# Optimization experiments

Measured on AMD Instinct MI355X. Metric: run time of the kernel, lower is better.

The kernel has to match this reference:

```python
import jax, jax.numpy as jnp
import numpy as np

HEADS = 16

def setup_inputs() -> dict:
    key = jax.random.key(0)
    ks = jax.random.split(key, 5)
    B, N, C = 2, 2048, 1024
    s = 0.02
    return {
        "x": jax.random.normal(ks[0], (B, N, C), jnp.float32),
        "y": jax.random.normal(ks[1], (B, N, C), jnp.float32),
        "w_qkv": jax.random.normal(ks[2], (C, 3 * C), jnp.float32) * s,  # acts as Linear weight^T
        "w_proj": jax.random.normal(ks[3], (C, C), jnp.float32) * s,
        "b_proj": jnp.zeros((C,), jnp.float32),
    }

def _qkv_heads(t, w_qkv, B, N, H, D):
    qkv = (t @ w_qkv).reshape(B, N, 3, H, D)
    qkv = jnp.transpose(qkv, (2, 0, 3, 1, 4))  # [3, B, H, N, D]
    return qkv[0], qkv[1], qkv[2]

def reference(x, y, w_qkv, w_proj, b_proj):
    B, N, C = x.shape
    H = HEADS
    D = C // H
    scale = D ** (-0.5)
    q, k, v = _qkv_heads(x, w_qkv, B, N, H, D)
    q1, k1, v1 = _qkv_heads(y, w_qkv, B, N, H, D)
    attn = jax.nn.softmax(jnp.einsum('bhnd,bhmd->bhnm', q, k) * scale, axis=-1)
    attn1 = jax.nn.softmax(jnp.einsum('bhnd,bhmd->bhnm', q1, k1) * scale, axis=-1)
    # cross-swapped values: x-branch attends over v1 (from y), y-branch over v (from x)
    ox = jnp.einsum('bhnm,bhmd->bhnd', attn, v1)
    oy = jnp.einsum('bhnm,bhmd->bhnd', attn1, v)
    ox = jnp.transpose(ox, (0, 2, 1, 3)).reshape(B, N, C)
    oy = jnp.transpose(oy, (0, 2, 1, 3)).reshape(B, N, C)
    x_out = ox @ w_proj + b_proj + x
    y_out = oy @ w_proj + b_proj + y
    return x_out, y_out
```

## Files before the change

kernel.cpp:

```cpp
#include <hip/hip_runtime.h>

using u16    = unsigned short;
using short8 = __attribute__((ext_vector_type(8))) short;
using f32x4  = __attribute__((ext_vector_type(4))) float;
using f32x16 = __attribute__((ext_vector_type(16))) float;

#define MFMA16(a, b, c) __builtin_amdgcn_mfma_f32_16x16x32_bf16(a, b, c, 0, 0, 0)
#define MFMA32(a, b, c) __builtin_amdgcn_mfma_f32_32x32x16_bf16(a, b, c, 0, 0, 0)

#define QSCALE 0.18033688011112042f

__device__ inline u16 f2bf(float f) {
  union { float f; unsigned u; } v; v.f = f;
  unsigned r = v.u + 0x7fffu + ((v.u >> 16) & 1u);
  return (u16)(r >> 16);
}

__device__ __forceinline__ void load_lds16(const u16* g, u16* l) {
  __builtin_amdgcn_global_load_lds((const __attribute__((address_space(1))) void*)g,
                                   (__attribute__((address_space(3))) void*)l, 16, 0, 0);
}

__device__ __forceinline__ unsigned cvt_pk_bf16(float lo, float hi) {
  unsigned r;
  asm("v_cvt_pk_bf16_f32 %0, %1, %2" : "=v"(r) : "v"(lo), "v"(hi));
  return r;
}

__device__ __forceinline__ void plswap(unsigned& a, unsigned& b) {
  auto r = __builtin_amdgcn_permlane32_swap(a, b, false, false);
  a = r[0];
  b = r[1];
}

__global__ __launch_bounds__(256) void cvt2_k(const float* __restrict__ s0,
                                              const float* __restrict__ s1,
                                              u16* __restrict__ d0,
                                              u16* __restrict__ d1) {
  const float* src = blockIdx.y ? s1 : s0;
  u16* dst = blockIdx.y ? d1 : d0;
  const int i = (blockIdx.x * 256 + threadIdx.x) * 8;
  const float4 a = *(const float4*)&src[i];
  const float4 b = *(const float4*)&src[i + 4];
  short8 o;
  o[0] = (short)f2bf(a.x); o[1] = (short)f2bf(a.y);
  o[2] = (short)f2bf(a.z); o[3] = (short)f2bf(a.w);
  o[4] = (short)f2bf(b.x); o[5] = (short)f2bf(b.y);
  o[6] = (short)f2bf(b.z); o[7] = (short)f2bf(b.w);
  *(short8*)&dst[i] = o;
}

__global__ __launch_bounds__(256) void cvtT_k(const float* __restrict__ src,
                                              u16* __restrict__ dst, int R, int C) {
  __shared__ float t[64][65];
  const int c0 = blockIdx.x * 64, r0 = blockIdx.y * 64;
  const int lc = threadIdx.x & 63, g = threadIdx.x >> 6;
#pragma unroll
  for (int i = 0; i < 16; ++i) {
    const int r = g + i * 4;
    t[r][lc] = src[(size_t)(r0 + r) * C + c0 + lc];
  }
  __syncthreads();
#pragma unroll
  for (int i = 0; i < 16; ++i) {
    const int c = g + i * 4;
    dst[(size_t)(c0 + c) * R + r0 + lc] = f2bf(t[lc][c]);
  }
}

template <int MODE>
__global__ __launch_bounds__(256, 4) void gemm_k(
    const u16* __restrict__ A0, const u16* __restrict__ A1,
    const u16* __restrict__ Bt,
    u16* __restrict__ q_out, u16* __restrict__ k_out, u16* __restrict__ v_out,
    float* __restrict__ c0, float* __restrict__ c1,
    const float* __restrict__ bias,
    const float* __restrict__ res0, const float* __restrict__ res1) {
  __shared__ alignas(16) u16 lA[128 * 64];
  __shared__ alignas(16) u16 lB[128 * 64];

  const int nx = (MODE == 0) ? 24 : 8;
  const int nb = nx * 32 * 2;
  const int bi = blockIdx.x;
  const int L  = (bi & 7) * (nb >> 3) + (bi >> 3);
  const int xt = L % nx;
  const int yt = (L / nx) & 31;
  const int z  = L / (nx * 32);

  const u16* A = z ? A1 : A0;
  float* c_out = z ? c1 : c0;
  const float* res = z ? res1 : res0;
  const int head_base = z * 32;

  const int tid = threadIdx.x;
  const int lane = tid & 63, wave = tid >> 6;
  const int quad = lane >> 4, l16 = lane & 15;
  const int lsw = (l16 & 7) * 8;
  const int wm = (wave >> 1) * 64, wn = (wave & 1) * 64;
  const int bn0 = xt * 128, bm0 = yt * 128;
  const int srow = lane >> 3;
  const int sg = (lane & 7) ^ srow;

  f32x4 acc[4][4] = {};

  for (int k0 = 0; k0 < 1024; k0 += 64) {
    __syncthreads();
#pragma unroll
    for (int it = 0; it < 4; ++it) {
      const int rb = wave * 32 + it * 8;
      const int r = rb + srow;
      load_lds16(&A[(size_t)(bm0 + r) * 1024 + k0 + sg * 8], &lA[rb * 64]);
      load_lds16(&Bt[(size_t)(bn0 + r) * 1024 + k0 + sg * 8], &lB[rb * 64]);
    }
    asm volatile("s_waitcnt vmcnt(0)" ::: "memory");
    __syncthreads();
#pragma unroll
    for (int kt = 0; kt < 2; ++kt) {
      short8 af[4], bfr[4];
#pragma unroll
      for (int i = 0; i < 4; ++i) {
        const int go = ((kt * 4 + quad) * 8) ^ lsw;
        af[i]  = *(const short8*)&lA[(wm + i * 16 + l16) * 64 + go];
        bfr[i] = *(const short8*)&lB[(wn + i * 16 + l16) * 64 + go];
      }
#pragma unroll
      for (int i = 0; i < 4; ++i)
#pragma unroll
        for (int j = 0; j < 4; ++j)
          acc[i][j] = MFMA16(af[i], bfr[j], acc[i][j]);
    }
  }

#pragma unroll
  for (int i = 0; i < 4; ++i) {
    const int row = bm0 + wm + i * 16 + quad * 4;
#pragma unroll
    for (int j = 0; j < 4; ++j) {
      const int col = bn0 + wn + j * 16 + l16;
      if (MODE == 0) {
        const int which = col >> 10;
        const int h = (col >> 6) & 15, d = col & 63;
        const int b = row >> 11, n0 = row & 2047;
        const size_t hh = (size_t)(head_base + b * 16 + h);
        if (which == 2) {
          union { u16 pk[4]; uint2 v; } u;
#pragma unroll
          for (int r = 0; r < 4; ++r) u.pk[r] = f2bf(acc[i][j][r]);
          *(uint2*)&v_out[(hh * 64 + d) * 2048 + n0] = u.v;
        } else if (which == 0) {
#pragma unroll
          for (int r = 0; r < 4; ++r)
            q_out[(hh * 2048 + n0 + r) * 64 + d] = f2bf(acc[i][j][r] * QSCALE);
        } else {
#pragma unroll
          for (int r = 0; r < 4; ++r)
            k_out[(hh * 2048 + n0 + r) * 64 + d] = f2bf(acc[i][j][r]);
        }
      } else {
#pragma unroll
        for (int r = 0; r < 4; ++r) {
          const int m = row + r;
          const size_t idx = (size_t)m * 1024 + col;
          c_out[idx] = acc[i][j][r] + bias[col] + res[idx];
        }
      }
    }
  }
}

__global__ __launch_bounds__(256, 4) void attn_k(const u16* __restrict__ Q,
                                                 const u16* __restrict__ K,
                                                 const u16* __restrict__ V,
                                                 u16* __restrict__ O) {
  __shared__ alignas(16) u16 kT[2][64 * 64];
  __shared__ alignas(16) u16 vT[2][64 * 64];

  const int tid = threadIdx.x;
  const int lane = tid & 63, wave = tid >> 6;
  const int qn = lane & 31, h = lane >> 5;

  const int d0 = blockIdx.x;
  const int swz = ((d0 & 7) << 7) | (d0 >> 3);
  const int qx = swz & 15;
  const int hh = (swz >> 4) & 15;
  const int z  = swz >> 8;
  const int s = z >> 1, b = z & 1;

  const int head_qk = z * 16 + hh;
  const int head_v  = (z ^ 2) * 16 + hh;
  const u16* Qh = Q + (size_t)head_qk * 2048 * 64;
  const u16* Kh = K + (size_t)head_qk * 2048 * 64;
  const u16* Vh = V + (size_t)head_v * 64 * 2048;
  const int qr0 = qx * 128 + wave * 32;

  short8 qf[4];
#pragma unroll
  for (int f = 0; f < 4; ++f)
    qf[f] = *(const short8*)&Qh[(size_t)(qr0 + qn) * 64 + f * 16 + h * 8];

  short8 ones;
#pragma unroll
  for (int j = 0; j < 8; ++j) ones[j] = (short)0x3F80;

  f32x16 oacc[2] = {};
  f32x16 lacc = {};

  const int srow = lane >> 3;

  union PU { unsigned u[4]; short8 s; };

  auto stage = [&](int buf, int j0) {
#pragma unroll
    for (int it = 0; it < 2; ++it) {
      const int rb = wave * 16 + it * 8;
      const int r = rb + srow;
      const int sgx = (lane & 7) ^ srow ^ (rb >> 3);
      load_lds16(&Kh[(size_t)(j0 + r) * 64 + sgx * 8], &kT[buf][rb * 64]);
      load_lds16(&Vh[(size_t)r * 2048 + j0 + sgx * 8], &vT[buf][rb * 64]);
    }
  };

  stage(0, 0);
  asm volatile("s_waitcnt vmcnt(0)" ::: "memory");
  __syncthreads();

  int cur = 0;
  for (int j0 = 0; j0 < 2048; j0 += 64) {
    if (j0 + 64 < 2048) stage(cur ^ 1, j0 + 64);
    const u16* kb = kT[cur];
    const u16* vb = vT[cur];

    PU pa[4];
#pragma unroll
    for (int t = 0; t < 2; ++t) {
      f32x16 sacc = {};
      const int row = t * 32 + qn;
      const int key = (row & 7) ^ (row >> 3);
#pragma unroll
      for (int kd = 0; kd < 4; ++kd) {
        const int go = ((kd * 2 + h) ^ key) * 8;
        const short8 kf = *(const short8*)&kb[row * 64 + go];
        sacc = MFMA32(kf, qf[kd], sacc);
      }

      unsigned pw[8];
#pragma unroll
      for (int j = 0; j < 8; ++j) {
        const float p0 = __builtin_amdgcn_exp2f(sacc[2 * j]);
        const float p1 = __builtin_amdgcn_exp2f(sacc[2 * j + 1]);
        pw[j] = cvt_pk_bf16(p0, p1);
      }

#pragma unroll
      for (int e = 0; e < 2; ++e) {
        unsigned a0 = pw[4 * e + 0], a2 = pw[4 * e + 2];
        unsigned a1 = pw[4 * e + 1], a3 = pw[4 * e + 3];
        plswap(a0, a2);
        plswap(a1, a3);
        pa[2 * t + e].u[0] = a0; pa[2 * t + e].u[1] = a1;
        pa[2 * t + e].u[2] = a2; pa[2 * t + e].u[3] = a3;
      }
    }

#pragma unroll
    for (int st = 0; st < 4; ++st)
      lacc = MFMA32(pa[st].s, ones, lacc);

#pragma unroll
    for (int dt = 0; dt < 2; ++dt) {
      const int row = dt * 32 + qn;
      const int key = (row & 7) ^ (row >> 3);
#pragma unroll
      for (int st = 0; st < 4; ++st) {
        const int go = ((st * 2 + h) ^ key) * 8;
        const short8 vf = *(const short8*)&vb[row * 64 + go];
        oacc[dt] = MFMA32(pa[st].s, vf, oacc[dt]);
      }
    }

    asm volatile("s_waitcnt vmcnt(0)" ::: "memory");
    __syncthreads();
    cur ^= 1;
  }

  u16* Ob = O + (size_t)s * 4096 * 1024;
#pragma unroll
  for (int r = 0; r < 16; ++r) {
    const int qrow = (r & 3) + 8 * (r >> 2) + 4 * h;
    const float inv = 1.f / lacc[r];
    const size_t base = (size_t)(b * 2048 + qr0 + qrow) * 1024 + hh * 64;
#pragma unroll
    for (int dt = 0; dt < 2; ++dt)
      Ob[base + dt * 32 + qn] = f2bf(oacc[dt][r] * inv);
  }
}

extern "C" void kernel_launch(void* const* d_in, const int* in_sizes, int n_in,
                              void* d_out, int out_size, void* d_ws, size_t ws_size,
                              hipStream_t stream) {
  const float* x      = (const float*)d_in[0];
  const float* y      = (const float*)d_in[1];
  const float* w_qkv  = (const float*)d_in[2];
  const float* w_proj = (const float*)d_in[3];
  const float* b_proj = (const float*)d_in[4];
  float* out = (float*)d_out;

  u16* xb     = (u16*)d_ws;
  u16* yb     = xb + 4194304;
  u16* Ob     = xb;
  u16* wqkvT  = yb + 4194304;
  u16* wprojT = wqkvT + 3145728;
  u16* Qs     = wprojT + 1048576;
  u16* Ks     = Qs + 8388608;
  u16* Vs     = Ks + 8388608;

  cvt2_k<<<dim3(2048, 2), 256, 0, stream>>>(x, y, xb, yb);
  cvtT_k<<<dim3(48, 16), 256, 0, stream>>>(w_qkv, wqkvT, 1024, 3072);
  cvtT_k<<<dim3(16, 16), 256, 0, stream>>>(w_proj, wprojT, 1024, 1024);

  gemm_k<0><<<1536, 256, 0, stream>>>(xb, yb, wqkvT, Qs, Ks, Vs,
                                      nullptr, nullptr, nullptr,
                                      nullptr, nullptr);

  attn_k<<<1024, 256, 0, stream>>>(Qs, Ks, Vs, Ob);

  gemm_k<1><<<512, 256, 0, stream>>>(Ob, Ob + 4194304, wprojT,
                                     nullptr, nullptr, nullptr,
                                     out, out + 4194304, b_proj, x, y);
}
```

Measured before the change: 263.8 us.

## Read K/V directly from global in attention and merge weight transpose launches

The attention kernel no longer stages K and V tiles into double-buffered shared memory with async global-to-LDS loads. Each wave now loads its MFMA fragments straight from global memory, which removes the barriers and waitcnts and frees LDS for occupancy. In exchange, the four waves of a block each fetch the same K/V data through cache, and there is no explicit prefetch overlap. The two weight transpose-convert launches are also merged into one 3D-grid launch to save a kernel launch.

```diff
diff --git a/kernel.cpp b/kernel.cpp
--- a/kernel.cpp
+++ b/kernel.cpp
@@ -50,8 +50,15 @@
   *(short8*)&dst[i] = o;
 }
 
-__global__ __launch_bounds__(256) void cvtT_k(const float* __restrict__ src,
-                                              u16* __restrict__ dst, int R, int C) {
+__global__ __launch_bounds__(256) void cvtT2_k(const float* __restrict__ s0,
+                                               u16* __restrict__ d0,
+                                               const float* __restrict__ s1,
+                                               u16* __restrict__ d1) {
+  const int z = blockIdx.z;
+  if (z && blockIdx.x >= 16) return;
+  const float* src = z ? s1 : s0;
+  u16* dst = z ? d1 : d0;
+  const int R = 1024, C = z ? 1024 : 3072;
   __shared__ float t[64][65];
   const int c0 = blockIdx.x * 64, r0 = blockIdx.y * 64;
   const int lc = threadIdx.x & 63, g = threadIdx.x >> 6;
@@ -172,9 +179,6 @@
                                                  const u16* __restrict__ K,
                                                  const u16* __restrict__ V,
                                                  u16* __restrict__ O) {
-  __shared__ alignas(16) u16 kT[2][64 * 64];
-  __shared__ alignas(16) u16 vT[2][64 * 64];
-
   const int tid = threadIdx.x;
   const int lane = tid & 63, wave = tid >> 6;
   const int qn = lane & 31, h = lane >> 5;
@@ -205,41 +209,18 @@
   f32x16 oacc[2] = {};
   f32x16 lacc = {};
 
-  const int srow = lane >> 3;
-
   union PU { unsigned u[4]; short8 s; };
 
-  auto stage = [&](int buf, int j0) {
-#pragma unroll
-    for (int it = 0; it < 2; ++it) {
-      const int rb = wave * 16 + it * 8;
-      const int r = rb + srow;
-      const int sgx = (lane & 7) ^ srow ^ (rb >> 3);
-      load_lds16(&Kh[(size_t)(j0 + r) * 64 + sgx * 8], &kT[buf][rb * 64]);
-      load_lds16(&Vh[(size_t)r * 2048 + j0 + sgx * 8], &vT[buf][rb * 64]);
-    }
-  };
-
-  stage(0, 0);
-  asm volatile("s_waitcnt vmcnt(0)" ::: "memory");
-  __syncthreads();
-
-  int cur = 0;
+#pragma unroll 1
   for (int j0 = 0; j0 < 2048; j0 += 64) {
-    if (j0 + 64 < 2048) stage(cur ^ 1, j0 + 64);
-    const u16* kb = kT[cur];
-    const u16* vb = vT[cur];
-
     PU pa[4];
 #pragma unroll
     for (int t = 0; t < 2; ++t) {
       f32x16 sacc = {};
-      const int row = t * 32 + qn;
-      const int key = (row & 7) ^ (row >> 3);
+      const int row = j0 + t * 32 + qn;
 #pragma unroll
       for (int kd = 0; kd < 4; ++kd) {
-        const int go = ((kd * 2 + h) ^ key) * 8;
-        const short8 kf = *(const short8*)&kb[row * 64 + go];
+        const short8 kf = *(const short8*)&Kh[(size_t)row * 64 + (kd * 2 + h) * 8];
         sacc = MFMA32(kf, qf[kd], sacc);
       }
 
@@ -268,19 +249,14 @@
 
 #pragma unroll
     for (int dt = 0; dt < 2; ++dt) {
-      const int row = dt * 32 + qn;
-      const int key = (row & 7) ^ (row >> 3);
+      const int drow = dt * 32 + qn;
 #pragma unroll
       for (int st = 0; st < 4; ++st) {
-        const int go = ((st * 2 + h) ^ key) * 8;
-        const short8 vf = *(const short8*)&vb[row * 64 + go];
+        const short8 vf =
+            *(const short8*)&Vh[(size_t)drow * 2048 + j0 + (st * 2 + h) * 8];
         oacc[dt] = MFMA32(pa[st].s, vf, oacc[dt]);
       }
     }
-
-    asm volatile("s_waitcnt vmcnt(0)" ::: "memory");
-    __syncthreads();
-    cur ^= 1;
   }
 
   u16* Ob = O + (size_t)s * 4096 * 1024;
@@ -315,8 +291,7 @@
   u16* Vs     = Ks + 8388608;
 
   cvt2_k<<<dim3(2048, 2), 256, 0, stream>>>(x, y, xb, yb);
-  cvtT_k<<<dim3(48, 16), 256, 0, stream>>>(w_qkv, wqkvT, 1024, 3072);
-  cvtT_k<<<dim3(16, 16), 256, 0, stream>>>(w_proj, wprojT, 1024, 1024);
+  cvtT2_k<<<dim3(48, 16, 2), 256, 0, stream>>>(w_qkv, wqkvT, w_proj, wprojT);
 
   gemm_k<0><<<1536, 256, 0, stream>>>(xb, yb, wqkvT, Qs, Ks, Vs,
                                       nullptr, nullptr, nullptr,
```

New measurement: 428.7 us. 62.5% more time.
